# Performance work log

Hardware: AMD Instinct MI355X
Metric: run time of the kernel (lower is better)

The kernel has to match this reference:

```python
import jax, jax.numpy as jnp
import numpy as np

N = 50000      # nodes per object type (2 types)
F = 128        # input feature dim (num_feat)
H = 64         # FLAGS.hidden1 == FLAGS.hidden2
E = 800000     # edges per relation
NET = 4        # edge types: (0,0),(0,1),(1,0),(1,1); for k: dst type i=k//2, src type j=k%2


def setup_inputs() -> dict:
    key = jax.random.key(0)
    ks = jax.random.split(key, 7)
    x0 = jax.random.normal(ks[0], (N, F), jnp.float32)
    x1 = jax.random.normal(ks[1], (N, F), jnp.float32)
    src = jax.random.randint(ks[2], (NET, E), 0, N, jnp.int32)
    dst = jax.random.randint(ks[3], (NET, E), 0, N, jnp.int32)
    # normalized adjacency values (~1/avg_degree keeps activations stable)
    ew = jax.random.uniform(ks[4], (NET, E), jnp.float32) / 16.0
    W1 = jax.random.normal(ks[5], (NET, F, H), jnp.float32) / np.sqrt(F).astype(np.float32)
    Wl = jax.random.normal(ks[6], (NET, NET, H, H), jnp.float32) / np.sqrt(H).astype(np.float32)
    return {"x0": x0, "x1": x1, "src": src, "dst": dst, "ew": ew, "W1": W1, "Wl": Wl}


def _spmm(src_k, dst_k, w_k, x):
    # sparse [N_i, N_j] adjacency @ dense x: gather + weighted scatter-add
    return jax.ops.segment_sum(w_k[:, None] * x[src_k], dst_k, num_segments=N)


def _layer(xs, Ws, src, dst, ew, relu):
    # xs: [x_type0, x_type1]; per edge type (i,j): out[i] += A_ij @ (x_j @ W_ij)
    outs = [jnp.zeros((N, Ws.shape[-1]), xs[0].dtype) for _ in range(2)]
    for k in range(NET):
        i, j = k // 2, k % 2
        outs[i] = outs[i] + _spmm(src[k], dst[k], ew[k], xs[j] @ Ws[k])
    if relu:
        outs = [jax.nn.relu(o) for o in outs]
    return outs


def reference(x0, x1, src, dst, ew, W1, Wl):
    h1 = _layer([x0, x1], W1, src, dst, ew, relu=True)       # hidden1
    e1 = _layer(h1, Wl[0], src, dst, ew, relu=True)          # embeddings1
    e2 = _layer(e1, Wl[1], src, dst, ew, relu=True)          # embeddings2
    e3 = _layer(e2, Wl[2], src, dst, ew, relu=True)          # embeddings3
    emb = _layer(e3, Wl[3], src, dst, ew, relu=False)        # embeddings = add_n(reltyp4), no relu
    # final concat per object type: [hidden1, embeddings1, embeddings] -> (N, 3H)
    return jnp.stack([jnp.concatenate([h1[t], e1[t], emb[t]], axis=1) for t in range(2)])
```

## Files before the change

kernel.cpp:

```cpp
#include <hip/hip_runtime.h>
#include <cstddef>

#define NREL 4
#define NSUP 2
#define HD 64
#define FD 128
#define BSHIFT 6
#define BUCKET 64
#define CHUNK 8192

static inline int idiv_up(int a, int b) { return (a + b - 1) / b; }

typedef __attribute__((ext_vector_type(8))) short bf16x8;
typedef __attribute__((ext_vector_type(4))) float f32x4;

__device__ __forceinline__ unsigned short f2bf(float f) {
    unsigned int u = __float_as_uint(f);
    unsigned int r = (u + 0x7FFFu + ((u >> 16) & 1u)) >> 16;
    return (unsigned short)r;
}
__device__ __forceinline__ float bflo(unsigned int v) {
    return __uint_as_float(v << 16);
}
__device__ __forceinline__ float bfhi(unsigned int v) {
    return __uint_as_float(v & 0xFFFF0000u);
}


__global__ void bhist_kernel(const int* __restrict__ dst, int* __restrict__ bhist,
                             int E2, int NBP) {
    int k = blockIdx.y;
    extern __shared__ int lh[];
    for (int i = threadIdx.x; i < NBP; i += blockDim.x) lh[i] = 0;
    __syncthreads();
    const int* dk = dst + (size_t)k * E2;
    for (int e = blockIdx.x * blockDim.x + threadIdx.x; e < E2; e += gridDim.x * blockDim.x)
        atomicAdd(&lh[dk[e] >> BSHIFT], 1);
    __syncthreads();
    int* bh = bhist + (size_t)k * NBP;
    for (int i = threadIdx.x; i < NBP; i += blockDim.x)
        if (lh[i]) atomicAdd(&bh[i], lh[i]);
}


__global__ void bscan_kernel(const int* __restrict__ bhist, int* __restrict__ bptr,
                             int* __restrict__ gcur, int NBP, int E2) {
    int k = blockIdx.x;
    __shared__ int wsum[16];
    int tid = threadIdx.x, wid = tid >> 6, lane = tid & 63;
    int v = (tid < NBP) ? bhist[(size_t)k * NBP + tid] : 0;
    int x = v;
    #pragma unroll
    for (int off = 1; off < 64; off <<= 1) {
        int y = __shfl_up(x, off, 64);
        if (lane >= off) x += y;
    }
    if (lane == 63) wsum[wid] = x;
    __syncthreads();
    if (wid == 0) {
        int s = (lane < 16) ? wsum[lane] : 0;
        #pragma unroll
        for (int off = 1; off < 16; off <<= 1) {
            int y = __shfl_up(s, off, 64);
            if (lane >= off) s += y;
        }
        if (lane < 16) wsum[lane] = s;
    }
    __syncthreads();
    int excl = x - v + (wid ? wsum[wid - 1] : 0);
    if (tid < NBP) {
        bptr[(size_t)k * (NBP + 1) + tid] = excl;
        gcur[(size_t)k * NBP + tid] = excl;
    }
    if (tid == 0) bptr[(size_t)k * (NBP + 1) + NBP] = E2;
}


__global__ void part_kernel(const int* __restrict__ src, const int* __restrict__ dst,
                            const float* __restrict__ ew, int* __restrict__ gcur,
                            int2* __restrict__ staged, int E, int E2, int N, int NBP) {
    int k = blockIdx.y;
    extern __shared__ int sh[];
    int* lcnt = sh;
    int* lbase = sh + NBP;
    for (int i = threadIdx.x; i < NBP; i += blockDim.x) lcnt[i] = 0;
    __syncthreads();
    const int* sk = src + (size_t)k * E2;
    const int* dk = dst + (size_t)k * E2;
    const float* wk = ew + (size_t)k * E2;
    int base = blockIdx.x * CHUNK;
    int n = min(CHUNK, E2 - base);
    for (int i = threadIdx.x; i < n; i += blockDim.x)
        atomicAdd(&lcnt[dk[base + i] >> BSHIFT], 1);
    __syncthreads();
    for (int i = threadIdx.x; i < NBP; i += blockDim.x) {
        int c = lcnt[i];
        lbase[i] = c ? atomicAdd(&gcur[(size_t)k * NBP + i], c) : 0;
    }
    __syncthreads();
    for (int i = threadIdx.x; i < NBP; i += blockDim.x) lcnt[i] = 0;
    __syncthreads();
    int2* out = staged + (size_t)k * E2;
    for (int i = threadIdx.x; i < n; i += blockDim.x) {
        int gi = base + i;
        int d = dk[gi];
        int b = d >> BSHIFT;
        int row = sk[gi] + ((gi >= E) ? N : 0);
        int local = atomicAdd(&lcnt[b], 1);
        out[lbase[b] + local] =
            make_int2(row | ((d & (BUCKET - 1)) << 17), __float_as_int(wk[gi]));
    }
}


__global__ void bsort_kernel(const int2* __restrict__ staged, const int* __restrict__ bptr,
                             int* __restrict__ rowptr, unsigned int* __restrict__ edges,
                             int E2, int N, int NBP) {
    int k = blockIdx.y;
    int b = blockIdx.x;
    __shared__ int hist[BUCKET];
    __shared__ int excl[BUCKET];
    __shared__ int cur[BUCKET];
    int tid = threadIdx.x;
    if (tid < BUCKET) hist[tid] = 0;
    __syncthreads();
    int beg = bptr[(size_t)k * (NBP + 1) + b];
    int end = bptr[(size_t)k * (NBP + 1) + b + 1];
    const int2* in = staged + (size_t)k * E2;
    for (int i = beg + tid; i < end; i += blockDim.x)
        atomicAdd(&hist[(in[i].x >> 17) & (BUCKET - 1)], 1);
    __syncthreads();
    if (tid < 64) {
        int v = hist[tid];
        int x = v;
        #pragma unroll
        for (int off = 1; off < 64; off <<= 1) {
            int y = __shfl_up(x, off, 64);
            if (tid >= off) x += y;
        }
        excl[tid] = x - v;
        cur[tid] = x - v;
    }
    __syncthreads();
    unsigned int* outp = edges + (size_t)k * E2;
    for (int i = beg + tid; i < end; i += blockDim.x) {
        int2 q = in[i];
        int dl = (q.x >> 17) & (BUCKET - 1);
        int pos = atomicAdd(&cur[dl], 1);
        unsigned int wb = (unsigned int)(f2bf(__int_as_float(q.y)) & 0x7FFF);
        outp[beg + pos] = ((unsigned int)q.x & 0x1FFFFu) | (wb << 17);
    }
    int node0 = b * BUCKET;
    if (tid < BUCKET && node0 + tid < N)
        rowptr[(size_t)k * (N + 1) + node0 + tid] = beg + excl[tid];
    if (b == 0 && tid == 0) rowptr[(size_t)k * (N + 1) + N] = E2;
}


__global__ void convx_kernel(const float* __restrict__ x0, const float* __restrict__ x1,
                             unsigned short* __restrict__ xb, int nq ) {
    for (int i = blockIdx.x * blockDim.x + threadIdx.x; i < 2 * nq;
         i += gridDim.x * blockDim.x) {
        const float4* xs = (i < nq) ? (const float4*)x0 : (const float4*)x1;
        int j = (i < nq) ? i : i - nq;
        float4 v = xs[j];
        ushort4 o;
        o.x = f2bf(v.x); o.y = f2bf(v.y); o.z = f2bf(v.z); o.w = f2bf(v.w);
        reinterpret_cast<ushort4*>(xb)[i] = o;
    }
}

__global__ void convw_kernel(const float* __restrict__ W, unsigned short* __restrict__ Wf,
                             int mats, int KK) {
    int tid = blockIdx.x * blockDim.x + threadIdx.x;
    int total = mats * KK * 4 * 64;
    if (tid >= total) return;
    int l = tid & 63;
    int n = (tid >> 6) & 3;
    int rest = tid >> 8;
    int kk = rest % KK;
    int mat = rest / KK;
    int h = l >> 4, c = l & 15;
    int K = KK * 32;
    const float* Wm = W + (size_t)mat * K * 64;
    unsigned short* o = Wf + (size_t)tid * 8;
    #pragma unroll
    for (int i = 0; i < 8; ++i)
        o[i] = f2bf(Wm[(size_t)(kk * 32 + h * 8 + i) * 64 + n * 16 + c]);
}


template <int K>
__global__ void gemm_mfma_kernel(const unsigned short* __restrict__ Xb,
                                 const unsigned short* __restrict__ Wf,
                                 unsigned short* __restrict__ Ybase, int N) {
    constexpr int KK = K / 32;
    int rel = blockIdx.y;
    const unsigned short* X = Xb + (size_t)(rel & 1) * N * K;
    const bf16x8* Wv = reinterpret_cast<const bf16x8*>(Wf + (size_t)rel * KK * 4 * 64 * 8);
    unsigned short* Y = Ybase + (size_t)rel * N * HD;
    int tid = threadIdx.x;
    int w = tid >> 6, l = tid & 63;
    int lr = l & 15, lh = l >> 4;
    int row0 = blockIdx.x * 128 + w * 32;
    f32x4 acc00 = {0.f,0.f,0.f,0.f}, acc01 = {0.f,0.f,0.f,0.f};
    f32x4 acc02 = {0.f,0.f,0.f,0.f}, acc03 = {0.f,0.f,0.f,0.f};
    f32x4 acc10 = {0.f,0.f,0.f,0.f}, acc11 = {0.f,0.f,0.f,0.f};
    f32x4 acc12 = {0.f,0.f,0.f,0.f}, acc13 = {0.f,0.f,0.f,0.f};
    int r0 = min(row0 + lr, N - 1);
    int r1 = min(row0 + 16 + lr, N - 1);
    const unsigned short* xp0 = X + (size_t)r0 * K + lh * 8;
    const unsigned short* xp1 = X + (size_t)r1 * K + lh * 8;
    #pragma unroll
    for (int kk = 0; kk < KK; ++kk) {
        bf16x8 a0 = *reinterpret_cast<const bf16x8*>(xp0 + kk * 32);
        bf16x8 a1 = *reinterpret_cast<const bf16x8*>(xp1 + kk * 32);
        bf16x8 b0 = Wv[(kk * 4 + 0) * 64 + l];
        bf16x8 b1 = Wv[(kk * 4 + 1) * 64 + l];
        bf16x8 b2 = Wv[(kk * 4 + 2) * 64 + l];
        bf16x8 b3 = Wv[(kk * 4 + 3) * 64 + l];
        acc00 = __builtin_amdgcn_mfma_f32_16x16x32_bf16(a0, b0, acc00, 0, 0, 0);
        acc01 = __builtin_amdgcn_mfma_f32_16x16x32_bf16(a0, b1, acc01, 0, 0, 0);
        acc02 = __builtin_amdgcn_mfma_f32_16x16x32_bf16(a0, b2, acc02, 0, 0, 0);
        acc03 = __builtin_amdgcn_mfma_f32_16x16x32_bf16(a0, b3, acc03, 0, 0, 0);
        acc10 = __builtin_amdgcn_mfma_f32_16x16x32_bf16(a1, b0, acc10, 0, 0, 0);
        acc11 = __builtin_amdgcn_mfma_f32_16x16x32_bf16(a1, b1, acc11, 0, 0, 0);
        acc12 = __builtin_amdgcn_mfma_f32_16x16x32_bf16(a1, b2, acc12, 0, 0, 0);
        acc13 = __builtin_amdgcn_mfma_f32_16x16x32_bf16(a1, b3, acc13, 0, 0, 0);
    }
    #pragma unroll
    for (int reg = 0; reg < 4; ++reg) {
        int rowa = row0 + lh * 4 + reg;
        if (rowa < N) {
            unsigned short* yp = Y + (size_t)rowa * HD + lr;
            yp[0]  = f2bf(acc00[reg]);
            yp[16] = f2bf(acc01[reg]);
            yp[32] = f2bf(acc02[reg]);
            yp[48] = f2bf(acc03[reg]);
        }
        int rowb = row0 + 16 + lh * 4 + reg;
        if (rowb < N) {
            unsigned short* yp = Y + (size_t)rowb * HD + lr;
            yp[0]  = f2bf(acc10[reg]);
            yp[16] = f2bf(acc11[reg]);
            yp[32] = f2bf(acc12[reg]);
            yp[48] = f2bf(acc13[reg]);
        }
    }
}


__global__ void spmm_kernel(const unsigned short* __restrict__ Ybase,
                            const int* __restrict__ rowptr, const unsigned int* __restrict__ edges,
                            unsigned short* __restrict__ act, float* __restrict__ outp,
                            int N, int E2, int relu) {
    int id = blockIdx.x;
    int g = id & 7;
    int t = g >> 2;
    int pbi = (id >> 3) * 4 + (g & 3);
    int wave = threadIdx.x >> 6;
    int lane = threadIdx.x & 63;
    int d = pbi * 4 + wave;
    if (d >= N) return;
    int h = lane >> 5;
    int c2 = (lane & 31) * 2;
    const unsigned short* Y = Ybase + (size_t)(2 * t) * N * HD;
    const unsigned int* ep = edges + (size_t)t * E2;
    int beg = rowptr[(size_t)t * (N + 1) + d];
    int end = rowptr[(size_t)t * (N + 1) + d + 1];
    float2 a[8];
    #pragma unroll
    for (int j = 0; j < 8; ++j) a[j] = make_float2(0.f, 0.f);
    if (beg < end) {
        int endm1 = end - 1;
        unsigned int m[8];
        #pragma unroll
        for (int j = 0; j < 8; ++j) {
            int idx = beg + 2 * j + h;
            m[j] = ep[idx < end ? idx : endm1];
        }
        for (int base = beg; ; ) {
            int nb = base + 16;
            bool more = nb < end;
            unsigned int n[8];
            if (more) {
                #pragma unroll
                for (int j = 0; j < 8; ++j) {
                    int idx = nb + 2 * j + h;
                    n[j] = ep[idx < end ? idx : endm1];
                }
            }
            #pragma unroll
            for (int j = 0; j < 8; ++j) {
                unsigned int q = m[j];
                unsigned int yv =
                    *reinterpret_cast<const unsigned int*>(Y + ((q & 0x1FFFFu) * HD + c2));
                float w = ((base + 2 * j + h) < end) ? __uint_as_float((q >> 17) << 16) : 0.f;
                a[j].x += w * bflo(yv);
                a[j].y += w * bfhi(yv);
            }
            if (!more) break;
            base = nb;
            #pragma unroll
            for (int j = 0; j < 8; ++j) m[j] = n[j];
        }
    }
    float2 s;
    s.x = ((a[0].x + a[1].x) + (a[2].x + a[3].x)) + ((a[4].x + a[5].x) + (a[6].x + a[7].x));
    s.y = ((a[0].y + a[1].y) + (a[2].y + a[3].y)) + ((a[4].y + a[5].y) + (a[6].y + a[7].y));
    s.x += __shfl_xor(s.x, 32, 64);
    s.y += __shfl_xor(s.y, 32, 64);
    if (relu) { s.x = fmaxf(s.x, 0.f); s.y = fmaxf(s.y, 0.f); }
    if (lane < 32) {
        if (act) {
            ushort2 ob; ob.x = f2bf(s.x); ob.y = f2bf(s.y);
            *reinterpret_cast<ushort2*>(&act[((size_t)t * N + d) * HD + c2]) = ob;
        }
        if (outp) *reinterpret_cast<float2*>(&outp[((size_t)t * N + d) * 192 + c2]) = s;
    }
}


extern "C" void kernel_launch(void* const* d_in, const int* in_sizes, int n_in,
                              void* d_out, int out_size, void* d_ws, size_t ws_size,
                              hipStream_t stream) {
    const float* x0 = (const float*)d_in[0];
    const float* x1 = (const float*)d_in[1];
    const int* src = (const int*)d_in[2];
    const int* dst = (const int*)d_in[3];
    const float* ew = (const float*)d_in[4];
    const float* W1 = (const float*)d_in[5];
    const float* Wl = (const float*)d_in[6];
    float* out = (float*)d_out;

    int N = in_sizes[0] / FD;
    int E = in_sizes[2] / NREL;
    int E2 = 2 * E;
    int NBP = idiv_up(N, BUCKET);

    char* ws = (char*)d_ws;
    size_t off = 0;
    auto alloc = [&](size_t bytes) -> void* {
        void* p = ws + off;
        off = (off + bytes + 255) & ~(size_t)255;
        return p;
    };
    int* bhist   = (int*)alloc((size_t)NSUP * NBP * 4);
    int* bptr    = (int*)alloc((size_t)NSUP * (NBP + 1) * 4);
    int* gcur    = (int*)alloc((size_t)NSUP * NBP * 4);
    int* rowptr  = (int*)alloc((size_t)NSUP * (N + 1) * 4);
    unsigned int* edges = (unsigned int*)alloc((size_t)NSUP * E2 * 4);
    unsigned short* y    = (unsigned short*)alloc((size_t)NREL * N * HD * 2);
    unsigned short* xb   = (unsigned short*)alloc((size_t)2 * N * FD * 2);
    unsigned short* actb = (unsigned short*)alloc((size_t)2 * N * HD * 2);
    unsigned short* W1f  = (unsigned short*)alloc((size_t)NREL * 4 * 4 * 64 * 8 * 2);
    unsigned short* Wlf  = (unsigned short*)alloc((size_t)16 * 2 * 4 * 64 * 8 * 2);
    int2* staged = (int2*)alloc((size_t)NSUP * E2 * 8);
    (void)ws_size;

    int nq = N * FD / 4;
    convx_kernel<<<2048, 256, 0, stream>>>(x0, x1, xb, nq);
    convw_kernel<<<idiv_up(NREL * 4 * 4 * 64, 256), 256, 0, stream>>>(W1, W1f, NREL, 4);
    convw_kernel<<<idiv_up(16 * 2 * 4 * 64, 256), 256, 0, stream>>>(Wl, Wlf, 16, 2);

    hipMemsetAsync(bhist, 0, (size_t)NSUP * NBP * 4, stream);
    dim3 egrid(idiv_up(E2, CHUNK), NSUP);
    bhist_kernel<<<egrid, 256, NBP * 4, stream>>>(dst, bhist, E2, NBP);
    bscan_kernel<<<NSUP, 1024, 0, stream>>>(bhist, bptr, gcur, NBP, E2);
    part_kernel<<<egrid, 256, 2 * NBP * 4, stream>>>(src, dst, ew, gcur, staged, E, E2, N, NBP);
    bsort_kernel<<<dim3(NBP, NSUP), 256, 0, stream>>>(staged, bptr, rowptr, edges, E2, N, NBP);

    dim3 ggrid(idiv_up(N, 128), NREL);
    int NB4 = idiv_up(N, 4);
    int sgx = idiv_up(NB4, 4) * 8;

    gemm_mfma_kernel<FD><<<ggrid, 256, 0, stream>>>(xb, W1f, y, N);
    spmm_kernel<<<sgx, 256, 0, stream>>>(y, rowptr, edges, actb, out + 0, N, E2, 1);

    for (int l = 0; l < 4; ++l) {
        gemm_mfma_kernel<HD><<<ggrid, 256, 0, stream>>>(
            actb, Wlf + (size_t)l * 4 * 2 * 4 * 64 * 8, y, N);
        float* op = (l == 0) ? (out + 64) : (l == 3) ? (out + 128) : nullptr;
        unsigned short* ap = (l == 3) ? nullptr : actb;
        int relu = (l == 3) ? 0 : 1;
        spmm_kernel<<<sgx, 256, 0, stream>>>(y, rowptr, edges, ap, op, N, E2, relu);
    }
}
```

Baseline: 511.7 us.

## Widen SpMM gathers to 8-byte loads and shrink partition chunk size

Each wave in the SpMM now covers a row with 16 lanes of 4 bf16 columns each, using 8-byte loads instead of 4-byte ones, and handles four edge groups per iteration. The final reduction uses two cross-lane shuffles. The partition kernel uses a smaller CHUNK, giving more blocks for the edge pass, and the histogram kernel is launched with a fixed grid. The goal is fewer, wider gather instructions and better parallelism during preprocessing, at the cost of a slightly longer reduction.

Result: faster. 485.5 us (-5.1%).

```diff
diff --git a/kernel.cpp b/kernel.cpp
--- a/kernel.cpp
+++ b/kernel.cpp
@@ -7,7 +7,7 @@
 #define FD 128
 #define BSHIFT 6
 #define BUCKET 64
-#define CHUNK 8192
+#define CHUNK 2048
 
 static inline int idiv_up(int a, int b) { return (a + b - 1) / b; }
 
@@ -262,61 +262,76 @@
     int lane = threadIdx.x & 63;
     int d = pbi * 4 + wave;
     if (d >= N) return;
-    int h = lane >> 5;
-    int c2 = (lane & 31) * 2;
+    int h = lane >> 4;
+    int c4 = (lane & 15) * 4;
     const unsigned short* Y = Ybase + (size_t)(2 * t) * N * HD;
     const unsigned int* ep = edges + (size_t)t * E2;
     int beg = rowptr[(size_t)t * (N + 1) + d];
     int end = rowptr[(size_t)t * (N + 1) + d + 1];
-    float2 a[8];
-    #pragma unroll
-    for (int j = 0; j < 8; ++j) a[j] = make_float2(0.f, 0.f);
+    float4 a0 = {0.f,0.f,0.f,0.f}, a1 = {0.f,0.f,0.f,0.f};
+    float4 a2 = {0.f,0.f,0.f,0.f}, a3 = {0.f,0.f,0.f,0.f};
     if (beg < end) {
         int endm1 = end - 1;
-        unsigned int m[8];
-        #pragma unroll
-        for (int j = 0; j < 8; ++j) {
-            int idx = beg + 2 * j + h;
-            m[j] = ep[idx < end ? idx : endm1];
+        unsigned int m0, m1, m2, m3;
+        {
+            int i0 = beg + 0 + h, i1 = beg + 4 + h, i2 = beg + 8 + h, i3 = beg + 12 + h;
+            m0 = ep[i0 < end ? i0 : endm1];
+            m1 = ep[i1 < end ? i1 : endm1];
+            m2 = ep[i2 < end ? i2 : endm1];
+            m3 = ep[i3 < end ? i3 : endm1];
         }
         for (int base = beg; ; ) {
             int nb = base + 16;
             bool more = nb < end;
-            unsigned int n[8];
+            unsigned int n0, n1, n2, n3;
             if (more) {
-                #pragma unroll
-                for (int j = 0; j < 8; ++j) {
-                    int idx = nb + 2 * j + h;
-                    n[j] = ep[idx < end ? idx : endm1];
-                }
+                int i0 = nb + 0 + h, i1 = nb + 4 + h, i2 = nb + 8 + h, i3 = nb + 12 + h;
+                n0 = ep[i0 < end ? i0 : endm1];
+                n1 = ep[i1 < end ? i1 : endm1];
+                n2 = ep[i2 < end ? i2 : endm1];
+                n3 = ep[i3 < end ? i3 : endm1];
             }
-            #pragma unroll
-            for (int j = 0; j < 8; ++j) {
-                unsigned int q = m[j];
-                unsigned int yv =
-                    *reinterpret_cast<const unsigned int*>(Y + ((q & 0x1FFFFu) * HD + c2));
-                float w = ((base + 2 * j + h) < end) ? __uint_as_float((q >> 17) << 16) : 0.f;
-                a[j].x += w * bflo(yv);
-                a[j].y += w * bfhi(yv);
-            }
+            uint2 y0 = *reinterpret_cast<const uint2*>(Y + ((m0 & 0x1FFFFu) * HD + c4));
+            uint2 y1 = *reinterpret_cast<const uint2*>(Y + ((m1 & 0x1FFFFu) * HD + c4));
+            uint2 y2 = *reinterpret_cast<const uint2*>(Y + ((m2 & 0x1FFFFu) * HD + c4));
+            uint2 y3 = *reinterpret_cast<const uint2*>(Y + ((m3 & 0x1FFFFu) * HD + c4));
+            float w0 = ((base + 0 + h) < end) ? __uint_as_float((m0 >> 17) << 16) : 0.f;
+            float w1 = ((base + 4 + h) < end) ? __uint_as_float((m1 >> 17) << 16) : 0.f;
+            float w2 = ((base + 8 + h) < end) ? __uint_as_float((m2 >> 17) << 16) : 0.f;
+            float w3 = ((base + 12 + h) < end) ? __uint_as_float((m3 >> 17) << 16) : 0.f;
+            a0.x += w0 * bflo(y0.x); a0.y += w0 * bfhi(y0.x);
+            a0.z += w0 * bflo(y0.y); a0.w += w0 * bfhi(y0.y);
+            a1.x += w1 * bflo(y1.x); a1.y += w1 * bfhi(y1.x);
+            a1.z += w1 * bflo(y1.y); a1.w += w1 * bfhi(y1.y);
+            a2.x += w2 * bflo(y2.x); a2.y += w2 * bfhi(y2.x);
+            a2.z += w2 * bflo(y2.y); a2.w += w2 * bfhi(y2.y);
+            a3.x += w3 * bflo(y3.x); a3.y += w3 * bfhi(y3.x);
+            a3.z += w3 * bflo(y3.y); a3.w += w3 * bfhi(y3.y);
             if (!more) break;
             base = nb;
-            #pragma unroll
-            for (int j = 0; j < 8; ++j) m[j] = n[j];
-        }
-    }
-    float2 s;
-    s.x = ((a[0].x + a[1].x) + (a[2].x + a[3].x)) + ((a[4].x + a[5].x) + (a[6].x + a[7].x));
-    s.y = ((a[0].y + a[1].y) + (a[2].y + a[3].y)) + ((a[4].y + a[5].y) + (a[6].y + a[7].y));
-    s.x += __shfl_xor(s.x, 32, 64);
-    s.y += __shfl_xor(s.y, 32, 64);
-    if (relu) { s.x = fmaxf(s.x, 0.f); s.y = fmaxf(s.y, 0.f); }
-    if (lane < 32) {
+            m0 = n0; m1 = n1; m2 = n2; m3 = n3;
+        }
+    }
+    float4 s;
+    s.x = (a0.x + a1.x) + (a2.x + a3.x);
+    s.y = (a0.y + a1.y) + (a2.y + a3.y);
+    s.z = (a0.z + a1.z) + (a2.z + a3.z);
+    s.w = (a0.w + a1.w) + (a2.w + a3.w);
+    s.x += __shfl_xor(s.x, 16, 64);  s.x += __shfl_xor(s.x, 32, 64);
+    s.y += __shfl_xor(s.y, 16, 64);  s.y += __shfl_xor(s.y, 32, 64);
+    s.z += __shfl_xor(s.z, 16, 64);  s.z += __shfl_xor(s.z, 32, 64);
+    s.w += __shfl_xor(s.w, 16, 64);  s.w += __shfl_xor(s.w, 32, 64);
+    if (relu) {
+        s.x = fmaxf(s.x, 0.f); s.y = fmaxf(s.y, 0.f);
+        s.z = fmaxf(s.z, 0.f); s.w = fmaxf(s.w, 0.f);
+    }
+    if (lane < 16) {
         if (act) {
-            ushort2 ob; ob.x = f2bf(s.x); ob.y = f2bf(s.y);
-            *reinterpret_cast<ushort2*>(&act[((size_t)t * N + d) * HD + c2]) = ob;
-        }
-        if (outp) *reinterpret_cast<float2*>(&outp[((size_t)t * N + d) * 192 + c2]) = s;
+            ushort4 ob;
+            ob.x = f2bf(s.x); ob.y = f2bf(s.y); ob.z = f2bf(s.z); ob.w = f2bf(s.w);
+            *reinterpret_cast<ushort4*>(&act[((size_t)t * N + d) * HD + c4]) = ob;
+        }
+        if (outp) *reinterpret_cast<float4*>(&outp[((size_t)t * N + d) * 192 + c4]) = s;
     }
 }
 
@@ -364,10 +379,10 @@
     convw_kernel<<<idiv_up(16 * 2 * 4 * 64, 256), 256, 0, stream>>>(Wl, Wlf, 16, 2);
 
     hipMemsetAsync(bhist, 0, (size_t)NSUP * NBP * 4, stream);
-    dim3 egrid(idiv_up(E2, CHUNK), NSUP);
-    bhist_kernel<<<egrid, 256, NBP * 4, stream>>>(dst, bhist, E2, NBP);
+    bhist_kernel<<<dim3(384, NSUP), 256, NBP * 4, stream>>>(dst, bhist, E2, NBP);
     bscan_kernel<<<NSUP, 1024, 0, stream>>>(bhist, bptr, gcur, NBP, E2);
-    part_kernel<<<egrid, 256, 2 * NBP * 4, stream>>>(src, dst, ew, gcur, staged, E, E2, N, NBP);
+    part_kernel<<<dim3(idiv_up(E2, CHUNK), NSUP), 256, 2 * NBP * 4, stream>>>(
+        src, dst, ew, gcur, staged, E, E2, N, NBP);
     bsort_kernel<<<dim3(NBP, NSUP), 256, 0, stream>>>(staged, bptr, rowptr, edges, E2, N, NBP);
 
     dim3 ggrid(idiv_up(N, 128), NREL);
```
